# Performance work log

Hardware: AMD Instinct MI355X
Metric: run time of the kernel (lower is better)

Reference implementation:

```python
import jax, jax.numpy as jnp
import numpy as np
from jax import lax

H = 2400
W = 2400
SX = 30
SY = 30
NBX = H // SX
NBY = W // SY
BANDS = 4
G = 0.5
PI = float(np.pi)


def setup_inputs() -> dict:
    key = jax.random.key(0)
    ks = jax.random.split(key, 11)
    f32 = jnp.float32
    return {
        "CHM": jax.random.normal(ks[0], (H, W), f32),
        "PATH1": jax.random.uniform(ks[1], (H, W), f32),
        "PATH2": jax.random.uniform(ks[2], (H, W), f32),
        "TH": jax.random.uniform(ks[3], (NBX, NBY), f32),
        "FAVD": jax.random.uniform(ks[4], (NBX, NBY), f32),
        "sza": jax.random.uniform(ks[5], (NBX, NBY), f32),
        "saa": jax.random.uniform(ks[6], (NBX, NBY), f32),
        "rl": jax.random.uniform(ks[7], (1, NBX, NBY), f32),
        "tl": jax.random.uniform(ks[8], (1, NBX, NBY), f32),
        "rs": jax.random.uniform(ks[9], (1, NBX, NBY), f32),
        "belta": jax.random.uniform(ks[10], (1, NBX, NBY), f32),
    }


def reference(CHM, PATH1, PATH2, TH, FAVD, sza, saa, rl, tl, rs, belta):
    # --- edge detection on binarized CHM (fixed 3x3 kernel, bias 8) ---
    mask = (CHM > 0).astype(jnp.float32)
    kern = jnp.array([[[[-1.0, -1.0, -1.0], [-1.0, 0.0, -1.0], [-1.0, -1.0, -1.0]]]], jnp.float32)
    inner = lax.conv_general_dilated(mask[None, None], kern, (1, 1), 'VALID')[0, 0] + 8.0
    edge = jnp.zeros((H, W), jnp.float32).at[1:-1, 1:-1].set(inner)
    edge = jnp.where(edge > 1.0, 1.0, 0.0)
    edge = jnp.where(mask == 0.0, 0.0, edge)
    tchm = jnp.where(mask > 0.0, 2.0, 0.0)  # 2=interior canopy, 0=gap
    tchm = jnp.where(edge == 1.0, 1.0, tchm)  # 1=edge pixel

    bsum = lambda x: x.reshape(NBX, SX, NBY, SY).sum(axis=(1, 3))
    count_edge = bsum(edge)             # [NBX,NBY]
    gap_count = bsum(2.0 - tchm) / 2.0  # [NBX,NBY]

    # --- block -> pixel nearest upsample (DynamicBlockUpsample2D) ---
    up = lambda p: jnp.repeat(jnp.repeat(p, SX, axis=0), SY, axis=1)
    FAVD_up = up(FAVD)
    TH_up = up(TH)
    sza_up = up(sza)

    # --- per-pixel Beer-Lambert gap probabilities (Single_k_nn_0303 recon) ---
    mu_pix = jnp.maximum(jnp.cos(sza_up * (PI / 180.0)), 1e-3)
    crown = jnp.maximum(CHM - TH_up, 0.0)  # within-crown depth
    gap_sun = jnp.exp(-G * FAVD_up * crown / mu_pix)
    gap_view = jnp.exp(-G * FAVD_up * crown)
    gap_p1 = jnp.exp(-G * FAVD_up * PATH1)
    gap_p2 = jnp.exp(-G * FAVD_up * PATH2)
    rel_h = CHM / CHM.max()
    chans = jnp.stack([gap_sun, gap_view, gap_p1, gap_p2, gap_sun * gap_view, mask,
                       gap_p1 * gap_p2, edge, crown, CHM, rel_h, edge * gap_sun,
                       mask * gap_view], axis=0)  # [13,H,W]
    te = chans.reshape(13, NBX, SX, NBY, SY).mean(axis=(2, 4))  # [13,NBX,NBY]

    # --- block-level k coefficients (cal_k recon) ---
    N = float(SX * SY)
    f_edge = count_edge / N
    f_gap = gap_count / N
    Pgs = te[0]
    Pboth = te[0] * te[1]

    # --- four-component BRF mix (BRF_nn recon) ---
    Kg = f_gap * Pgs                       # sunlit ground
    Kz = f_gap * (1.0 - Pgs)               # shaded ground
    Kc = (1.0 - f_gap) * Pboth             # sunlit crown
    Kt = jnp.maximum((1.0 - f_gap) - Kc, 0.0)  # shaded crown
    hot = 1.0 + 0.1 * jnp.cos(saa * (PI / 180.0))
    brf = (rl * Kc + tl * belta * Kt + rs * Kg + rs * belta * Kz
           + rl * te[7] * te[10] + tl * (1.0 - belta) * te[11] + rs * te[12] * f_gap)
    brf = brf * hot  # [1,NBX,NBY]
    return jnp.broadcast_to(brf, (BANDS, NBX, NBY))
```

## Files before the change

kernel.cpp:

```cpp
#include <hip/hip_runtime.h>
#include <math.h>

#define H 2400
#define W 2400
#define SX 30
#define SY 30
#define NBX 80
#define NBY 80
#define NBLK (NBX * NBY)
#define GCOEF 0.5f
#define PI_F 3.14159265358979323846f

__global__ __launch_bounds__(256) void block_stats(
    const float* __restrict__ chm,
    const float* __restrict__ th,
    const float* __restrict__ favd,
    const float* __restrict__ sza,
    float* __restrict__ sums)
{
    __shared__ float tile[32][33];
    __shared__ float red[4][8];

    const int blk = blockIdx.x;
    const int bx = blk / NBY, by = blk % NBY;
    const int gi0 = bx * SX, gj0 = by * SY;
    const int tid = threadIdx.x;

    for (int idx = tid; idx < 32 * 32; idx += 256) {
        int r = idx >> 5, c = idx & 31;
        int gi = gi0 - 1 + r, gj = gj0 - 1 + c;
        float v = 0.0f;
        if (gi >= 0 && gi < H && gj >= 0 && gj < W) v = chm[gi * W + gj];
        tile[r][c] = v;
    }
    __syncthreads();

    const float th_b   = th[blk];
    const float favd_b = favd[blk];
    const float sza_b  = sza[blk];
    const float a      = -GCOEF * favd_b;
    const float mu     = fmaxf(cosf(sza_b * (PI_F / 180.0f)), 1e-3f);
    const float inv_mu = 1.0f / mu;

    float s_mask = 0.f, s_edge = 0.f, s_gs = 0.f, s_gv = 0.f;
    float s_chm = 0.f, s_egs = 0.f, s_mgv = 0.f;
    float vmax = -INFINITY;

    for (int idx = tid; idx < SX * SY; idx += 256) {
        int li = idx / SY, lj = idx - li * SY;
        int r = li + 1, c = lj + 1;
        float center = tile[r][c];
        bool  m = center > 0.0f;
        int gi = gi0 + li, gj = gj0 + lj;
        int ns = 0;
        ns += (tile[r - 1][c - 1] > 0.f);
        ns += (tile[r - 1][c    ] > 0.f);
        ns += (tile[r - 1][c + 1] > 0.f);
        ns += (tile[r    ][c - 1] > 0.f);
        ns += (tile[r    ][c + 1] > 0.f);
        ns += (tile[r + 1][c - 1] > 0.f);
        ns += (tile[r + 1][c    ] > 0.f);
        ns += (tile[r + 1][c + 1] > 0.f);
        bool interior = (gi >= 1) & (gi <= H - 2) & (gj >= 1) & (gj <= W - 2);
        float edge = (m && interior && (ns <= 6)) ? 1.0f : 0.0f;

        float crown    = fmaxf(center - th_b, 0.0f);
        float gap_view = __expf(a * crown);
        float gap_sun  = __expf(a * crown * inv_mu);
        float fm = m ? 1.0f : 0.0f;

        s_mask += fm;
        s_edge += edge;
        s_gs   += gap_sun;
        s_gv   += gap_view;
        s_chm  += center;
        s_egs  += edge * gap_sun;
        s_mgv  += fm * gap_view;
        vmax = fmaxf(vmax, center);
    }

    for (int off = 32; off >= 1; off >>= 1) {
        s_mask += __shfl_down(s_mask, off, 64);
        s_edge += __shfl_down(s_edge, off, 64);
        s_gs   += __shfl_down(s_gs,   off, 64);
        s_gv   += __shfl_down(s_gv,   off, 64);
        s_chm  += __shfl_down(s_chm,  off, 64);
        s_egs  += __shfl_down(s_egs,  off, 64);
        s_mgv  += __shfl_down(s_mgv,  off, 64);
        vmax = fmaxf(vmax, __shfl_down(vmax, off, 64));
    }
    int wid = tid >> 6, lane = tid & 63;
    if (lane == 0) {
        red[wid][0] = s_mask; red[wid][1] = s_edge; red[wid][2] = s_gs;
        red[wid][3] = s_gv;   red[wid][4] = s_chm;  red[wid][5] = s_egs;
        red[wid][6] = s_mgv;  red[wid][7] = vmax;
    }
    __syncthreads();
    if (tid < 8) {
        float t;
        if (tid == 7) {
            t = fmaxf(fmaxf(red[0][7], red[1][7]), fmaxf(red[2][7], red[3][7]));
        } else {
            t = red[0][tid] + red[1][tid] + red[2][tid] + red[3][tid];
        }
        sums[tid * NBLK + blk] = t;
    }
}

__global__ __launch_bounds__(1024) void finalize_all(
    const float* __restrict__ sums,
    const float* __restrict__ saa,
    const float* __restrict__ rl,
    const float* __restrict__ tl,
    const float* __restrict__ rs,
    const float* __restrict__ belta,
    float* __restrict__ out)
{
    __shared__ float smax[16];
    const int tid = threadIdx.x;

    float m = -INFINITY;
    for (int b = tid; b < NBLK; b += 1024) m = fmaxf(m, sums[7 * NBLK + b]);
    for (int off = 32; off >= 1; off >>= 1) m = fmaxf(m, __shfl_down(m, off, 64));
    int wid = tid >> 6, lane = tid & 63;
    if (lane == 0) smax[wid] = m;
    __syncthreads();
    if (tid == 0) {
        float t = smax[0];
        for (int w2 = 1; w2 < 16; ++w2) t = fmaxf(t, smax[w2]);
        smax[0] = t;
    }
    __syncthreads();
    const float inv_max = 1.0f / smax[0];
    const float invN = 1.0f / 900.0f;

    for (int b = tid; b < NBLK; b += 1024) {
        float s_mask = sums[0 * NBLK + b];
        float s_edge = sums[1 * NBLK + b];
        float te0  = sums[2 * NBLK + b] * invN;
        float te1  = sums[3 * NBLK + b] * invN;
        float s_chm = sums[4 * NBLK + b];
        float te11 = sums[5 * NBLK + b] * invN;
        float te12 = sums[6 * NBLK + b] * invN;

        float te10 = s_chm * invN * inv_max;
        float te7  = s_edge * invN;
        float f_gap = ((900.0f - s_mask) + 0.5f * s_edge) * invN;

        float Pgs   = te0;
        float Pboth = te0 * te1;
        float Kg = f_gap * Pgs;
        float Kz = f_gap * (1.0f - Pgs);
        float Kc = (1.0f - f_gap) * Pboth;
        float Kt = fmaxf((1.0f - f_gap) - Kc, 0.0f);
        float hot = 1.0f + 0.1f * cosf(saa[b] * (PI_F / 180.0f));

        float brf = (rl[b] * Kc + tl[b] * belta[b] * Kt + rs[b] * Kg
                   + rs[b] * belta[b] * Kz + rl[b] * te7 * te10
                   + tl[b] * (1.0f - belta[b]) * te11
                   + rs[b] * te12 * f_gap) * hot;

        out[0 * NBLK + b] = brf;
        out[1 * NBLK + b] = brf;
        out[2 * NBLK + b] = brf;
        out[3 * NBLK + b] = brf;
    }
}

extern "C" void kernel_launch(void* const* d_in, const int* in_sizes, int n_in,
                              void* d_out, int out_size, void* d_ws, size_t ws_size,
                              hipStream_t stream) {
    const float* chm   = (const float*)d_in[0];
    const float* th    = (const float*)d_in[3];
    const float* favd  = (const float*)d_in[4];
    const float* sza   = (const float*)d_in[5];
    const float* saa   = (const float*)d_in[6];
    const float* rl    = (const float*)d_in[7];
    const float* tl    = (const float*)d_in[8];
    const float* rs    = (const float*)d_in[9];
    const float* belta = (const float*)d_in[10];
    float* out = (float*)d_out;

    float* sums = (float*)d_ws;

    block_stats<<<NBLK, 256, 0, stream>>>(chm, th, favd, sza, sums);
    finalize_all<<<1, 1024, 0, stream>>>(sums, saa, rl, tl, rs, belta, out);
}
```

Measured before the change: 136.0 us.

## Process four adjacent blocks per workgroup with one wave per block

Each workgroup now loads a 32x122 halo tile covering four horizontally adjacent 30x30 blocks, and each 64-lane wave reduces one block by itself. This cuts the redundant halo loads and the number of workgroups, and removes the cross-wave shared-memory reduction and its barrier. The sums workspace layout also changes to per-block AoS so the finalize kernel can read it with two float4 loads. In exchange each wave has less parallelism per block (64 lanes over 900 pixels), and there are only 1600 workgroups.

```diff
diff --git a/kernel.cpp b/kernel.cpp
--- a/kernel.cpp
+++ b/kernel.cpp
@@ -18,22 +18,27 @@
     const float* __restrict__ sza,
     float* __restrict__ sums)
 {
-    __shared__ float tile[32][33];
-    __shared__ float red[4][8];
+    __shared__ float tile[32 * 123];
 
-    const int blk = blockIdx.x;
-    const int bx = blk / NBY, by = blk % NBY;
-    const int gi0 = bx * SX, gj0 = by * SY;
+    const int bx    = blockIdx.x / (NBY / 4);
+    const int bcol4 = blockIdx.x % (NBY / 4);
+    const int gi0 = bx * SX;
+    const int gj0 = bcol4 * (4 * SY);
     const int tid = threadIdx.x;
 
-    for (int idx = tid; idx < 32 * 32; idx += 256) {
-        int r = idx >> 5, c = idx & 31;
+    for (int idx = tid; idx < 32 * 122; idx += 256) {
+        int r = idx / 122, c = idx - r * 122;
         int gi = gi0 - 1 + r, gj = gj0 - 1 + c;
         float v = 0.0f;
         if (gi >= 0 && gi < H && gj >= 0 && gj < W) v = chm[gi * W + gj];
-        tile[r][c] = v;
+        tile[r * 123 + c] = v;
     }
     __syncthreads();
+
+    const int w    = tid >> 6;
+    const int lane = tid & 63;
+    const int blk  = bx * NBY + bcol4 * 4 + w;
+    const int cw   = w * SY;
 
     const float th_b   = th[blk];
     const float favd_b = favd[blk];
@@ -46,21 +51,16 @@
     float s_chm = 0.f, s_egs = 0.f, s_mgv = 0.f;
     float vmax = -INFINITY;
 
-    for (int idx = tid; idx < SX * SY; idx += 256) {
-        int li = idx / SY, lj = idx - li * SY;
-        int r = li + 1, c = lj + 1;
-        float center = tile[r][c];
+    for (int p = lane; p < SX * SY; p += 64) {
+        int li = p / SY, lj = p - li * SY;
+        const float* row = &tile[(li + 1) * 123 + cw + lj + 1];
+        float center = row[0];
         bool  m = center > 0.0f;
-        int gi = gi0 + li, gj = gj0 + lj;
         int ns = 0;
-        ns += (tile[r - 1][c - 1] > 0.f);
-        ns += (tile[r - 1][c    ] > 0.f);
-        ns += (tile[r - 1][c + 1] > 0.f);
-        ns += (tile[r    ][c - 1] > 0.f);
-        ns += (tile[r    ][c + 1] > 0.f);
-        ns += (tile[r + 1][c - 1] > 0.f);
-        ns += (tile[r + 1][c    ] > 0.f);
-        ns += (tile[r + 1][c + 1] > 0.f);
+        ns += (row[-124] > 0.f); ns += (row[-123] > 0.f); ns += (row[-122] > 0.f);
+        ns += (row[-1]   > 0.f); ns += (row[1]    > 0.f);
+        ns += (row[122]  > 0.f); ns += (row[123]  > 0.f); ns += (row[124]  > 0.f);
+        int gi = gi0 + li, gj = gj0 + cw + lj;
         bool interior = (gi >= 1) & (gi <= H - 2) & (gj >= 1) & (gj <= W - 2);
         float edge = (m && interior && (ns <= 6)) ? 1.0f : 0.0f;
 
@@ -89,21 +89,10 @@
         s_mgv  += __shfl_down(s_mgv,  off, 64);
         vmax = fmaxf(vmax, __shfl_down(vmax, off, 64));
     }
-    int wid = tid >> 6, lane = tid & 63;
     if (lane == 0) {
-        red[wid][0] = s_mask; red[wid][1] = s_edge; red[wid][2] = s_gs;
-        red[wid][3] = s_gv;   red[wid][4] = s_chm;  red[wid][5] = s_egs;
-        red[wid][6] = s_mgv;  red[wid][7] = vmax;
-    }
-    __syncthreads();
-    if (tid < 8) {
-        float t;
-        if (tid == 7) {
-            t = fmaxf(fmaxf(red[0][7], red[1][7]), fmaxf(red[2][7], red[3][7]));
-        } else {
-            t = red[0][tid] + red[1][tid] + red[2][tid] + red[3][tid];
-        }
-        sums[tid * NBLK + blk] = t;
+        float* o = &sums[blk * 8];
+        o[0] = s_mask; o[1] = s_edge; o[2] = s_gs;  o[3] = s_gv;
+        o[4] = s_chm;  o[5] = s_egs;  o[6] = s_mgv; o[7] = vmax;
     }
 }
 
@@ -120,7 +109,7 @@
     const int tid = threadIdx.x;
 
     float m = -INFINITY;
-    for (int b = tid; b < NBLK; b += 1024) m = fmaxf(m, sums[7 * NBLK + b]);
+    for (int b = tid; b < NBLK; b += 1024) m = fmaxf(m, sums[b * 8 + 7]);
     for (int off = 32; off >= 1; off >>= 1) m = fmaxf(m, __shfl_down(m, off, 64));
     int wid = tid >> 6, lane = tid & 63;
     if (lane == 0) smax[wid] = m;
@@ -135,13 +124,15 @@
     const float invN = 1.0f / 900.0f;
 
     for (int b = tid; b < NBLK; b += 1024) {
-        float s_mask = sums[0 * NBLK + b];
-        float s_edge = sums[1 * NBLK + b];
-        float te0  = sums[2 * NBLK + b] * invN;
-        float te1  = sums[3 * NBLK + b] * invN;
-        float s_chm = sums[4 * NBLK + b];
-        float te11 = sums[5 * NBLK + b] * invN;
-        float te12 = sums[6 * NBLK + b] * invN;
+        float4 lo = *(const float4*)&sums[b * 8];
+        float4 hi = *(const float4*)&sums[b * 8 + 4];
+        float s_mask = lo.x;
+        float s_edge = lo.y;
+        float te0  = lo.z * invN;
+        float te1  = lo.w * invN;
+        float s_chm = hi.x;
+        float te11 = hi.y * invN;
+        float te12 = hi.z * invN;
 
         float te10 = s_chm * invN * inv_max;
         float te7  = s_edge * invN;
@@ -183,6 +174,6 @@
 
     float* sums = (float*)d_ws;
 
-    block_stats<<<NBLK, 256, 0, stream>>>(chm, th, favd, sza, sums);
+    block_stats<<<NBX * (NBY / 4), 256, 0, stream>>>(chm, th, favd, sza, sums);
     finalize_all<<<1, 1024, 0, stream>>>(sums, saa, rl, tl, rs, belta, out);
 }
```

Result: no change. 134.0 us (-1.5%).
